# Performance work log

Hardware: AMD Instinct MI355X
Metric: run time of the kernel (lower is better)

The kernel has to match this reference:

```python
import jax, jax.numpy as jnp
import numpy as np
from jax import lax


def _conv(x, w):
    # x: [B,H,W,C], w: [kh,kw,Cin,Cout], stride 1, 'same' padding
    return lax.conv_general_dilated(x, w, window_strides=(1, 1), padding='SAME',
                                    dimension_numbers=('NHWC', 'HWIO', 'NHWC'))


def setup_inputs() -> dict:
    key = jax.random.key(0)
    ks = jax.random.split(key, 4)
    B, T, H, W, Cin, F = 16, 5, 256, 256, 3, 8
    return {
        'input_tensor': jax.random.normal(ks[0], (B, T, H, W, Cin), jnp.float32),
        'kernel': jax.random.normal(ks[1], (3, 3, Cin, 4 * F), jnp.float32) * 0.1,
        'recurrent_kernel': jax.random.normal(ks[2], (3, 3, F, 4 * F), jnp.float32) * 0.1,
        'bias': jnp.zeros((4 * F,), jnp.float32),
        'gamma': jnp.ones((F,), jnp.float32),
        'beta': jnp.zeros((F,), jnp.float32),
        'moving_mean': jnp.zeros((F,), jnp.float32),
        'moving_var': jnp.ones((F,), jnp.float32),
        'dense_w': jax.random.normal(ks[3], (F, 2), jnp.float32) * 0.1,
        'dense_b': jnp.zeros((2,), jnp.float32),
    }


def reference(input_tensor, kernel, recurrent_kernel, bias, gamma, beta,
              moving_mean, moving_var, dense_w, dense_b):
    B, T, H, W, Cin = input_tensor.shape
    F = recurrent_kernel.shape[2]
    xs = jnp.moveaxis(input_tensor, 1, 0)  # [T,B,H,W,Cin] time-major for scan
    h0 = jnp.zeros((B, H, W, F), input_tensor.dtype)

    def step(carry, x_t):
        h, c = carry
        # fused 4-gate pre-activations, Keras gate order: i, f, c(g), o
        z = _conv(x_t, kernel) + _conv(h, recurrent_kernel) + bias
        i, f, g, o = jnp.split(z, 4, axis=-1)
        i = jax.nn.sigmoid(i)
        f = jax.nn.sigmoid(f)
        g = jnp.tanh(g)
        o = jax.nn.sigmoid(o)
        c = f * c + i * g
        h = o * jnp.tanh(c)
        return (h, c), None

    (h, _), _ = lax.scan(step, (h0, h0), xs)  # return_sequences=False -> last h

    # BatchNormalization (inference, Keras eps=1e-3)
    eps = 1e-3
    x = (h - moving_mean) * lax.rsqrt(moving_var + eps) * gamma + beta
    # LeakyReLU, Keras default alpha=0.3
    x = jnp.where(x >= 0, x, 0.3 * x)
    # Dense(2) over channel dim
    return jnp.einsum('bhwf,fk->bhwk', x, dense_w) + dense_b
```

## Files before the change

### kernel.cpp

```cpp
#include <hip/hip_runtime.h>


#define BB  16
#define TT  5
#define HH  256
#define WW  256
#define CIN 3
#define FF  8
#define GG  32

#define TW  32
#define THT 16
#define LW  34
#define LH  18
#define NG  8

#define SW  30
#define SH  14
#define NPX 9
#define NPY 19

#define LOG2E 1.44269504088896340736f

typedef _Float16 half8  __attribute__((ext_vector_type(8)));
typedef _Float16 half4  __attribute__((ext_vector_type(4)));
typedef _Float16 half2t __attribute__((ext_vector_type(2)));
typedef float    floatx4 __attribute__((ext_vector_type(4)));

__device__ __forceinline__ float frcp(float x) { return __builtin_amdgcn_rcpf(x); }
__device__ __forceinline__ float sig2(float z)  { return frcp(1.0f + __builtin_amdgcn_exp2f(z)); }
__device__ __forceinline__ float tanh2(float z) { return 1.0f - 2.0f * frcp(1.0f + __builtin_amdgcn_exp2f(z)); }

__device__ __forceinline__ int clampi(int v, int lo, int hi) {
    return v < lo ? lo : (v > hi ? hi : v);
}

#define MFMA(A, B, C) __builtin_amdgcn_mfma_f32_16x16x32_f16((A), (B), (C), 0, 0, 0)

#define GATES(ACC0, ACC1, C0, C1, CN0, CN1, HN0, HN1)                         \
  float CN0, CN1, HN0, HN1;                                                   \
  {                                                                           \
    float s0 = lo8 ? ACC0[2] : ACC0[0]; float r0 = __shfl_xor(s0, 8, 64);     \
    float s1 = lo8 ? ACC0[3] : ACC0[1]; float r1 = __shfl_xor(s1, 8, 64);     \
    float s2 = lo8 ? ACC1[2] : ACC1[0]; float r2 = __shfl_xor(s2, 8, 64);     \
    float s3 = lo8 ? ACC1[3] : ACC1[1]; float r3 = __shfl_xor(s3, 8, 64);     \
    const float zi0 = lo8 ? ACC0[0] : r0, zi1 = lo8 ? ACC0[1] : r1;           \
    const float zf0 = lo8 ? r0 : ACC0[2], zf1 = lo8 ? r1 : ACC0[3];           \
    const float zg0 = lo8 ? ACC1[0] : r2, zg1 = lo8 ? ACC1[1] : r3;           \
    const float zo0 = lo8 ? r2 : ACC1[2], zo1 = lo8 ? r3 : ACC1[3];           \
    const float ii0 = sig2(zi0), ff0 = sig2(zf0), gg0 = tanh2(zg0), oo0 = sig2(zo0); \
    CN0 = ff0 * (C0) + ii0 * gg0;                                             \
    HN0 = oo0 * tanh2(CN0 * (2.0f * LOG2E));                                  \
    const float ii1 = sig2(zi1), ff1 = sig2(zf1), gg1 = tanh2(zg1), oo1 = sig2(zo1); \
    CN1 = ff1 * (C1) + ii1 * gg1;                                             \
    HN1 = oo1 * tanh2(CN1 * (2.0f * LOG2E));                                  \
  }

__global__ void build_frags(const float* __restrict__ wk,
                            const float* __restrict__ wr,
                            _Float16* __restrict__ blob) {
    const int lane = threadIdx.x & 63;
    const int quad = lane >> 4, nlo = lane & 15;
    for (int chunk = 0; chunk < 5; ++chunk) {
        for (int nh = 0; nh < 2; ++nh) {
            const int n = nh * 16 + nlo;
            const float scale = (n >= 16 && n < 24) ? (2.0f * LOG2E) : (-LOG2E);
            const int frag = chunk * 2 + nh;
            _Float16* dhi = blob + ((size_t)frag * 64 + lane) * 8;
            _Float16* dlo = (chunk >= 2)
                ? blob + ((size_t)(10 + (chunk - 2) * 2 + nh) * 64 + lane) * 8
                : nullptr;
            for (int j = 0; j < 8; ++j) {
                const int k = quad * 8 + j;
                float w = 0.0f;
                if (chunk == 0) {
                    int tap = k >> 2, ci = k & 3;
                    if (ci < 3) w = wk[(tap * 3 + ci) * GG + n];
                } else if (chunk == 1) {
                    if (quad == 0 && j < 3) w = wk[(8 * 3 + j) * GG + n];
                } else {
                    int c = chunk - 2;
                    int tap = c * 4 + quad, ci = j;
                    if (tap < 9) w = wr[(tap * FF + ci) * GG + n];
                }
                w *= scale;
                _Float16 wh = (_Float16)w;
                dhi[j] = wh;
                if (dlo) dlo[j] = (_Float16)(w - (float)wh);
            }
        }
    }
}

template <int FIRSTPAIR>
__global__ __launch_bounds__(256) void lstm_pair(
    const float* __restrict__ xg,
    int t,
    const _Float16* __restrict__ blob,
    const float* __restrict__ bias,
    const _Float16* __restrict__ hin,
    _Float16* __restrict__ hout,
    const _Float16* __restrict__ cin,
    _Float16* __restrict__ cout)
{
    __shared__ half8 hls1[LH * LW];
    __shared__ half4 xls1[LH * LW];
    __shared__ half4 xls2[THT * TW];
    __shared__ __align__(16) _Float16 hls2[THT * TW * FF];

    const int tid  = threadIdx.x;
    const int lane = tid & 63, wave = tid >> 6;
    const int quad = lane >> 4, nlo = lane & 15;
    const bool lo8 = (nlo < 8);
    const int fc = nlo & 7;
    const int m0 = quad * 4 + (lo8 ? 0 : 2);

    const int bx = blockIdx.x, by = blockIdx.y, b = blockIdx.z;
    const int x0 = bx * SW - 1, y0 = by * SH - 1;

    half8 bfh[10], bfl[6];
#pragma unroll
    for (int i = 0; i < 10; ++i)
        bfh[i] = *(const half8*)(blob + ((size_t)i * 64 + lane) * 8);
#pragma unroll
    for (int i = 0; i < 6; ++i)
        bfl[i] = *(const half8*)(blob + ((size_t)(10 + i) * 64 + lane) * 8);

    const float bv0 = bias[nlo] * (-LOG2E);
    const float bv1 = bias[16 + nlo] * (lo8 ? 2.0f * LOG2E : -LOG2E);

    float xr1[3][3];
    bool  xin1[3];
#pragma unroll
    for (int k = 0; k < 3; ++k) {
        const int l = tid + k * 256;
        const bool in = (l < LH * LW);
        xin1[k] = in;
        int r = l / LW, c = l - r * LW;
        int gy = y0 - 1 + r, gx = x0 - 1 + c;
        const bool inb = in && (unsigned)gy < HH && (unsigned)gx < WW;
        const float* p = xg + (((size_t)(b * TT + t) * HH + gy) * WW + gx) * CIN;
        xr1[k][0] = inb ? p[0] : 0.0f;
        xr1[k][1] = inb ? p[1] : 0.0f;
        xr1[k][2] = inb ? p[2] : 0.0f;
    }
    float xr2[2][3];
#pragma unroll
    for (int k = 0; k < 2; ++k) {
        const int l = tid + k * 256;
        int r = l >> 5, c = l & 31;
        int gy = y0 + r, gx = x0 + c;
        const bool inb = (unsigned)gy < HH && (unsigned)gx < WW;
        const float* p = xg + (((size_t)(b * TT + t + 1) * HH + gy) * WW + gx) * CIN;
        xr2[k][0] = inb ? p[0] : 0.0f;
        xr2[k][1] = inb ? p[1] : 0.0f;
        xr2[k][2] = inb ? p[2] : 0.0f;
    }
    half8 hr[3];
    if (!FIRSTPAIR) {
#pragma unroll
        for (int k = 0; k < 3; ++k) {
            const int l = tid + k * 256;
            const bool in = (l < LH * LW);
            int r = l / LW, c = l - r * LW;
            int gy = y0 - 1 + r, gx = x0 - 1 + c;
            const bool inb = in && (unsigned)gy < HH && (unsigned)gx < WW;
            half8 v = {(_Float16)0, (_Float16)0, (_Float16)0, (_Float16)0,
                       (_Float16)0, (_Float16)0, (_Float16)0, (_Float16)0};
            if (inb) v = *(const half8*)(hin + ((size_t)(b * HH + gy) * WW + gx) * FF);
            hr[k] = v;
        }
    }
    half2t cpre[NG];
    if (!FIRSTPAIR) {
#pragma unroll
        for (int g = 0; g < NG; ++g) {
            const int lr  = wave * 4 + (g >> 1);
            const int gx0 = (g & 1) * 16;
            const int gy  = y0 + lr;
            const int gxa = x0 + gx0 + m0;
            const bool iny = (unsigned)gy < HH;
            half2t cv; cv.x = (_Float16)0; cv.y = (_Float16)0;
            const _Float16* cp = cin + ((size_t)(b * HH + gy) * WW + gxa) * FF + fc;
            if (iny && (unsigned)gxa < WW)       cv.x = cp[0];
            if (iny && (unsigned)(gxa + 1) < WW) cv.y = cp[FF];
            cpre[g] = cv;
        }
    }

#pragma unroll
    for (int k = 0; k < 3; ++k) {
        if (xin1[k]) {
            half4 vh;
            vh.x = (_Float16)xr1[k][0];
            vh.y = (_Float16)xr1[k][1];
            vh.z = (_Float16)xr1[k][2];
            vh.w = (_Float16)0;
            xls1[tid + k * 256] = vh;
        }
    }
#pragma unroll
    for (int k = 0; k < 2; ++k) {
        half4 vh;
        vh.x = (_Float16)xr2[k][0];
        vh.y = (_Float16)xr2[k][1];
        vh.z = (_Float16)xr2[k][2];
        vh.w = (_Float16)0;
        xls2[tid + k * 256] = vh;
    }
    if (!FIRSTPAIR) {
#pragma unroll
        for (int k = 0; k < 3; ++k)
            if (xin1[k]) hls1[tid + k * 256] = hr[k];
    }
    __syncthreads();

    half2t creg[NG];
#pragma unroll
    for (int g = 0; g < NG; ++g) {
        const int lr  = wave * 4 + (g >> 1);
        const int gx0 = (g & 1) * 16;
        const int lc  = gx0 + nlo;

        const int t0 = 2 * quad, t1 = t0 + 1;
        half4 p  = xls1[(lr + t0 / 3) * LW + lc + t0 % 3];
        half4 q  = xls1[(lr + t1 / 3) * LW + lc + t1 % 3];
        half4 s8 = xls1[(lr + 2) * LW + lc + 2];
        half8 a_xA = (half8){p.x, p.y, p.z, p.w, q.x, q.y, q.z, q.w};
        half8 a_xB = (half8){s8.x, s8.y, s8.z, s8.w, s8.x, s8.y, s8.z, s8.w};

        floatx4 acc0 = {bv0, bv0, bv0, bv0};
        floatx4 acc1 = {bv1, bv1, bv1, bv1};
        acc0 = MFMA(a_xA, bfh[0], acc0);  acc1 = MFMA(a_xA, bfh[1], acc1);
        acc0 = MFMA(a_xB, bfh[2], acc0);  acc1 = MFMA(a_xB, bfh[3], acc1);
        if (!FIRSTPAIR) {
#pragma unroll
            for (int c = 0; c < 3; ++c) {
                int tap = c * 4 + quad;
                if (tap > 8) tap = 8;
                half8 ah = hls1[(lr + tap / 3) * LW + lc + tap % 3];
                acc0 = MFMA(ah, bfh[4 + c * 2], acc0);
                acc1 = MFMA(ah, bfh[5 + c * 2], acc1);
                acc0 = MFMA(ah, bfl[c * 2 + 0], acc0);
                acc1 = MFMA(ah, bfl[c * 2 + 1], acc1);
            }
        }

        const float c0 = FIRSTPAIR ? 0.0f : (float)cpre[g].x;
        const float c1 = FIRSTPAIR ? 0.0f : (float)cpre[g].y;
        GATES(acc0, acc1, c0, c1, cn0, cn1, hn0, hn1);

        half2t cc; cc.x = (_Float16)cn0; cc.y = (_Float16)cn1;
        creg[g] = cc;

        const int gy   = y0 + lr;
        const int colm = gx0 + m0;
        const int gxa  = x0 + colm;
        const bool iny = (unsigned)gy < HH;
        _Float16 h0v = (_Float16)hn0, h1v = (_Float16)hn1;
        if (!(iny && (unsigned)gxa < WW))       h0v = (_Float16)0;
        if (!(iny && (unsigned)(gxa + 1) < WW)) h1v = (_Float16)0;
        hls2[(lr * TW + colm) * FF + fc]     = h0v;
        hls2[(lr * TW + colm + 1) * FF + fc] = h1v;
    }
    __syncthreads();

#pragma unroll
    for (int g = 0; g < NG; ++g) {
        const int lr  = wave * 4 + (g >> 1);
        const int gx0 = (g & 1) * 16;
        const int lc  = gx0 + nlo;

        const int t0 = 2 * quad, t1 = t0 + 1;
        half4 p  = xls2[clampi(lr + t0 / 3 - 1, 0, THT - 1) * TW + clampi(lc + t0 % 3 - 1, 0, TW - 1)];
        half4 q  = xls2[clampi(lr + t1 / 3 - 1, 0, THT - 1) * TW + clampi(lc + t1 % 3 - 1, 0, TW - 1)];
        half4 s8 = xls2[clampi(lr + 1, 0, THT - 1) * TW + clampi(lc + 1, 0, TW - 1)];
        half8 a_xA = (half8){p.x, p.y, p.z, p.w, q.x, q.y, q.z, q.w};
        half8 a_xB = (half8){s8.x, s8.y, s8.z, s8.w, s8.x, s8.y, s8.z, s8.w};

        floatx4 acc0 = {bv0, bv0, bv0, bv0};
        floatx4 acc1 = {bv1, bv1, bv1, bv1};
        acc0 = MFMA(a_xA, bfh[0], acc0);  acc1 = MFMA(a_xA, bfh[1], acc1);
        acc0 = MFMA(a_xB, bfh[2], acc0);  acc1 = MFMA(a_xB, bfh[3], acc1);
#pragma unroll
        for (int c = 0; c < 3; ++c) {
            int tap = c * 4 + quad;
            if (tap > 8) tap = 8;
            const int rr = clampi(lr + tap / 3 - 1, 0, THT - 1);
            const int cc = clampi(lc + tap % 3 - 1, 0, TW - 1);
            half8 ah = *(const half8*)(hls2 + (rr * TW + cc) * FF);
            acc0 = MFMA(ah, bfh[4 + c * 2], acc0);
            acc1 = MFMA(ah, bfh[5 + c * 2], acc1);
            acc0 = MFMA(ah, bfl[c * 2 + 0], acc0);
            acc1 = MFMA(ah, bfl[c * 2 + 1], acc1);
        }

        GATES(acc0, acc1, (float)creg[g].x, (float)creg[g].y, cn0, cn1, hn0, hn1);

        const int gy   = y0 + lr;
        const int colm = gx0 + m0;
        const int gxa  = x0 + colm;
        const bool rowok = (lr >= 1) && (lr <= SH) && ((unsigned)gy < HH);
        const bool c0ok = rowok && (colm >= 1) && (colm <= SW) && ((unsigned)gxa < WW);
        const bool c1ok = rowok && (colm + 1 <= SW) && ((unsigned)(gxa + 1) < WW);
        const size_t base = ((size_t)(b * HH + gy) * WW + gxa) * FF + fc;
        if (c0ok) {
            hout[base] = (_Float16)hn0;
            cout[base] = (_Float16)cn0;
        }
        if (c1ok) {
            hout[base + FF] = (_Float16)hn1;
            cout[base + FF] = (_Float16)cn1;
        }
    }
}

__global__ __launch_bounds__(256) void lstm_last(
    const float* __restrict__ xg,
    const _Float16* __restrict__ blob,
    const float* __restrict__ bias,
    const _Float16* __restrict__ hin,
    const _Float16* __restrict__ cin,
    const float* __restrict__ gamma, const float* __restrict__ beta,
    const float* __restrict__ mean,  const float* __restrict__ var,
    const float* __restrict__ dw,    const float* __restrict__ db,
    float* __restrict__ out)
{
    __shared__ half8 hls[LH * LW];
    __shared__ half4 xls[LH * LW];

    const int tid  = threadIdx.x;
    const int lane = tid & 63, wave = tid >> 6;
    const int quad = lane >> 4, nlo = lane & 15;
    const bool lo8 = (nlo < 8);
    const int fc = nlo & 7;
    const int m0 = quad * 4 + (lo8 ? 0 : 2);
    const int bx = blockIdx.x, by = blockIdx.y, b = blockIdx.z;
    const int t = TT - 1;

    half8 bfh[10], bfl[6];
#pragma unroll
    for (int i = 0; i < 10; ++i)
        bfh[i] = *(const half8*)(blob + ((size_t)i * 64 + lane) * 8);
#pragma unroll
    for (int i = 0; i < 6; ++i)
        bfl[i] = *(const half8*)(blob + ((size_t)(10 + i) * 64 + lane) * 8);

    const float bv0 = bias[nlo] * (-LOG2E);
    const float bv1 = bias[16 + nlo] * (lo8 ? 2.0f * LOG2E : -LOG2E);

    float xr[3][3];
    bool  xin[3];
#pragma unroll
    for (int k = 0; k < 3; ++k) {
        const int l = tid + k * 256;
        const bool in = (l < LH * LW);
        xin[k] = in;
        int r = l / LW, c = l - r * LW;
        int gy = by * THT + r - 1, gx = bx * TW + c - 1;
        const bool inb = in && (unsigned)gy < HH && (unsigned)gx < WW;
        const float* p = xg + (((size_t)(b * TT + t) * HH + gy) * WW + gx) * CIN;
        xr[k][0] = inb ? p[0] : 0.0f;
        xr[k][1] = inb ? p[1] : 0.0f;
        xr[k][2] = inb ? p[2] : 0.0f;
    }
    half8 hr[3];
#pragma unroll
    for (int k = 0; k < 3; ++k) {
        const int l = tid + k * 256;
        const bool in = (l < LH * LW);
        int r = l / LW, c = l - r * LW;
        int gy = by * THT + r - 1, gx = bx * TW + c - 1;
        const bool inb = in && (unsigned)gy < HH && (unsigned)gx < WW;
        half8 v = {(_Float16)0, (_Float16)0, (_Float16)0, (_Float16)0,
                   (_Float16)0, (_Float16)0, (_Float16)0, (_Float16)0};
        if (inb) v = *(const half8*)(hin + ((size_t)(b * HH + gy) * WW + gx) * FF);
        hr[k] = v;
    }
    half2t cpre[NG];
#pragma unroll
    for (int g = 0; g < NG; ++g) {
        const int lr  = wave * 4 + (g >> 1);
        const int gx0 = (g & 1) * 16;
        const int gy  = by * THT + lr;
        const int gxa = bx * TW + gx0 + m0;
        const _Float16* cp = cin + ((size_t)(b * HH + gy) * WW + gxa) * FF + fc;
        half2t cv; cv.x = cp[0]; cv.y = cp[FF];
        cpre[g] = cv;
    }

#pragma unroll
    for (int k = 0; k < 3; ++k) {
        if (xin[k]) {
            half4 vh;
            vh.x = (_Float16)xr[k][0];
            vh.y = (_Float16)xr[k][1];
            vh.z = (_Float16)xr[k][2];
            vh.w = (_Float16)0;
            xls[tid + k * 256] = vh;
            hls[tid + k * 256] = hr[k];
        }
    }
    __syncthreads();

    const float bn_s = gamma[fc] * rsqrtf(var[fc] + 1e-3f);
    const float bn_b = beta[fc] - mean[fc] * bn_s;
    const float dw0 = dw[fc * 2 + 0], dw1 = dw[fc * 2 + 1];
    const float db0 = db[0], db1 = db[1];

#pragma unroll
    for (int g = 0; g < NG; ++g) {
        const int lr  = wave * 4 + (g >> 1);
        const int gx0 = (g & 1) * 16;
        const int lc  = gx0 + nlo;

        const int t0 = 2 * quad, t1 = t0 + 1;
        half4 p  = xls[(lr + t0 / 3) * LW + lc + t0 % 3];
        half4 q  = xls[(lr + t1 / 3) * LW + lc + t1 % 3];
        half4 s8 = xls[(lr + 2) * LW + lc + 2];
        half8 a_xA = (half8){p.x, p.y, p.z, p.w, q.x, q.y, q.z, q.w};
        half8 a_xB = (half8){s8.x, s8.y, s8.z, s8.w, s8.x, s8.y, s8.z, s8.w};

        floatx4 acc0 = {bv0, bv0, bv0, bv0};
        floatx4 acc1 = {bv1, bv1, bv1, bv1};
        acc0 = MFMA(a_xA, bfh[0], acc0);  acc1 = MFMA(a_xA, bfh[1], acc1);
        acc0 = MFMA(a_xB, bfh[2], acc0);  acc1 = MFMA(a_xB, bfh[3], acc1);
#pragma unroll
        for (int c = 0; c < 3; ++c) {
            int tap = c * 4 + quad;
            if (tap > 8) tap = 8;
            half8 ah = hls[(lr + tap / 3) * LW + lc + tap % 3];
            acc0 = MFMA(ah, bfh[4 + c * 2], acc0);
            acc1 = MFMA(ah, bfh[5 + c * 2], acc1);
            acc0 = MFMA(ah, bfl[c * 2 + 0], acc0);
            acc1 = MFMA(ah, bfl[c * 2 + 1], acc1);
        }

        GATES(acc0, acc1, (float)cpre[g].x, (float)cpre[g].y, cn0, cn1, hn0, hn1);
        (void)cn0; (void)cn1;

        const int gy = by * THT + lr;
        float y0 = bn_s * hn0 + bn_b; y0 = (y0 >= 0.f) ? y0 : 0.3f * y0;
        float y1 = bn_s * hn1 + bn_b; y1 = (y1 >= 0.f) ? y1 : 0.3f * y1;
        float p00 = y0 * dw0, p01 = y0 * dw1;
        float p10 = y1 * dw0, p11 = y1 * dw1;
#pragma unroll
        for (int m = 1; m <= 4; m <<= 1) {
            p00 += __shfl_xor(p00, m, 64);
            p01 += __shfl_xor(p01, m, 64);
            p10 += __shfl_xor(p10, m, 64);
            p11 += __shfl_xor(p11, m, 64);
        }
        const int j = nlo & 7;
        if (j < 4) {
            const int px = m0 + (j >> 1);
            const int k  = j & 1;
            float val = (j == 0 ? p00 : j == 1 ? p01 : j == 2 ? p10 : p11)
                        + (k ? db1 : db0);
            out[((size_t)(b * HH + gy) * WW + bx * TW + gx0 + px) * 2 + k] = val;
        }
    }
}

extern "C" void kernel_launch(void* const* d_in, const int* in_sizes, int n_in,
                              void* d_out, int out_size, void* d_ws, size_t ws_size,
                              hipStream_t stream) {
    const float* x     = (const float*)d_in[0];
    const float* wk    = (const float*)d_in[1];
    const float* wr    = (const float*)d_in[2];
    const float* bias  = (const float*)d_in[3];
    const float* gamma = (const float*)d_in[4];
    const float* beta  = (const float*)d_in[5];
    const float* mean  = (const float*)d_in[6];
    const float* var   = (const float*)d_in[7];
    const float* dw    = (const float*)d_in[8];
    const float* db    = (const float*)d_in[9];
    float* out = (float*)d_out;

    const size_t state = (size_t)BB * HH * WW * FF;
    _Float16* blob = (_Float16*)d_ws;
    _Float16* hA = (_Float16*)((char*)d_ws + 32768);
    _Float16* hB = hA + state;
    _Float16* cA = hB + state;
    _Float16* cB = cA + state;

    build_frags<<<1, 64, 0, stream>>>(wk, wr, blob);

    dim3 pgrid(NPX, NPY, BB), block(256);
    lstm_pair<1><<<pgrid, block, 0, stream>>>(x, 0, blob, bias,
                                              nullptr, hA, nullptr, cA);
    lstm_pair<0><<<pgrid, block, 0, stream>>>(x, 2, blob, bias,
                                              hA, hB, cA, cB);
    dim3 lgrid(WW / TW, HH / THT, BB);
    lstm_last<<<lgrid, block, 0, stream>>>(x, blob, bias, hB, cB,
                                           gamma, beta, mean, var, dw, db, out);
}
```

Baseline: 292.4 us.

## Switch LSTM kernels to single-wave 16x16 tiles and drop block barriers

Each fused LSTM kernel now uses one 64-lane wave per block instead of four waves. Tiles shrink from 32x16 to 16x16, with an 18x18 haloed load and a stride of 14 for the pair kernels. Because all LDS producers and consumers sit in one wave, the __syncthreads calls are removed, and each lane walks 16 rows sequentially with the cell state kept in registers. The cost is a larger share of redundant halo recomputation and many more small blocks. It also leans on in-wave LDS ordering, with no explicit barrier or fence.

New measurement: 287.7 us. No clear change (-1.6%).

```diff
diff --git a/kernel.cpp b/kernel.cpp
--- a/kernel.cpp
+++ b/kernel.cpp
@@ -9,16 +9,10 @@
 #define FF  8
 #define GG  32
 
-#define TW  32
-#define THT 16
-#define LW  34
-#define LH  18
-#define NG  8
-
-#define SW  30
-#define SH  14
-#define NPX 9
-#define NPY 19
+#define TIW 16
+#define TLW 18
+#define STR 14
+#define NPT 19
 
 #define LOG2E 1.44269504088896340736f
 
@@ -93,7 +87,7 @@
 }
 
 template <int FIRSTPAIR>
-__global__ __launch_bounds__(256) void lstm_pair(
+__global__ __launch_bounds__(64) void lstm_pair(
     const float* __restrict__ xg,
     int t,
     const _Float16* __restrict__ blob,
@@ -103,20 +97,19 @@
     const _Float16* __restrict__ cin,
     _Float16* __restrict__ cout)
 {
-    __shared__ half8 hls1[LH * LW];
-    __shared__ half4 xls1[LH * LW];
-    __shared__ half4 xls2[THT * TW];
-    __shared__ __align__(16) _Float16 hls2[THT * TW * FF];
-
-    const int tid  = threadIdx.x;
-    const int lane = tid & 63, wave = tid >> 6;
+    __shared__ half4 xls1[TLW * TLW];
+    __shared__ half8 hls1[TLW * TLW];
+    __shared__ half4 xls2[TIW * TIW];
+    __shared__ __align__(16) _Float16 hls2[TIW * TIW * FF];
+
+    const int lane = threadIdx.x;
     const int quad = lane >> 4, nlo = lane & 15;
     const bool lo8 = (nlo < 8);
     const int fc = nlo & 7;
     const int m0 = quad * 4 + (lo8 ? 0 : 2);
 
     const int bx = blockIdx.x, by = blockIdx.y, b = blockIdx.z;
-    const int x0 = bx * SW - 1, y0 = by * SH - 1;
+    const int x0 = bx * STR - 1, y0 = by * STR - 1;
 
     half8 bfh[10], bfl[6];
 #pragma unroll
@@ -129,103 +122,133 @@
     const float bv0 = bias[nlo] * (-LOG2E);
     const float bv1 = bias[16 + nlo] * (lo8 ? 2.0f * LOG2E : -LOG2E);
 
-    float xr1[3][3];
-    bool  xin1[3];
-#pragma unroll
-    for (int k = 0; k < 3; ++k) {
-        const int l = tid + k * 256;
-        const bool in = (l < LH * LW);
-        xin1[k] = in;
-        int r = l / LW, c = l - r * LW;
-        int gy = y0 - 1 + r, gx = x0 - 1 + c;
+    float xr1[6][3];
+#pragma unroll
+    for (int k = 0; k < 6; ++k) {
+        const int l = lane + k * 64;
+        const bool in = (l < TLW * TLW);
+        const int r = l / TLW, c = l - r * TLW;
+        const int gy = y0 - 1 + r, gx = x0 - 1 + c;
         const bool inb = in && (unsigned)gy < HH && (unsigned)gx < WW;
         const float* p = xg + (((size_t)(b * TT + t) * HH + gy) * WW + gx) * CIN;
         xr1[k][0] = inb ? p[0] : 0.0f;
         xr1[k][1] = inb ? p[1] : 0.0f;
         xr1[k][2] = inb ? p[2] : 0.0f;
     }
-    float xr2[2][3];
-#pragma unroll
-    for (int k = 0; k < 2; ++k) {
-        const int l = tid + k * 256;
-        int r = l >> 5, c = l & 31;
-        int gy = y0 + r, gx = x0 + c;
+    half8 hr[6];
+    if (!FIRSTPAIR) {
+#pragma unroll
+        for (int k = 0; k < 6; ++k) {
+            const int l = lane + k * 64;
+            const bool in = (l < TLW * TLW);
+            const int r = l / TLW, c = l - r * TLW;
+            const int gy = y0 - 1 + r, gx = x0 - 1 + c;
+            const bool inb = in && (unsigned)gy < HH && (unsigned)gx < WW;
+            half8 v = {(_Float16)0, (_Float16)0, (_Float16)0, (_Float16)0,
+                       (_Float16)0, (_Float16)0, (_Float16)0, (_Float16)0};
+            if (inb) v = *(const half8*)(hin + ((size_t)(b * HH + gy) * WW + gx) * FF);
+            hr[k] = v;
+        }
+    }
+    half2t creg[TIW];
+#pragma unroll
+    for (int g = 0; g < TIW; ++g) {
+        half2t cv; cv.x = (_Float16)0; cv.y = (_Float16)0;
+        if (!FIRSTPAIR) {
+            const int gy = y0 + g, gxa = x0 + m0;
+            const bool iny = (unsigned)gy < HH;
+            const _Float16* cp = cin + ((size_t)(b * HH + gy) * WW + gxa) * FF + fc;
+            if (iny && (unsigned)gxa < WW)       cv.x = cp[0];
+            if (iny && (unsigned)(gxa + 1) < WW) cv.y = cp[FF];
+        }
+        creg[g] = cv;
+    }
+
+#pragma unroll
+    for (int k = 0; k < 6; ++k) {
+        const int l = lane + k * 64;
+        if (l < TLW * TLW) {
+            half4 vh;
+            vh.x = (_Float16)xr1[k][0];
+            vh.y = (_Float16)xr1[k][1];
+            vh.z = (_Float16)xr1[k][2];
+            vh.w = (_Float16)0;
+            xls1[l] = vh;
+            if (!FIRSTPAIR) hls1[l] = hr[k];
+        }
+    }
+
+    float xr2[4][3];
+#pragma unroll
+    for (int k = 0; k < 4; ++k) {
+        const int l = lane + k * 64;
+        const int r = l >> 4, c = l & 15;
+        const int gy = y0 + r, gx = x0 + c;
         const bool inb = (unsigned)gy < HH && (unsigned)gx < WW;
         const float* p = xg + (((size_t)(b * TT + t + 1) * HH + gy) * WW + gx) * CIN;
         xr2[k][0] = inb ? p[0] : 0.0f;
         xr2[k][1] = inb ? p[1] : 0.0f;
         xr2[k][2] = inb ? p[2] : 0.0f;
     }
-    half8 hr[3];
-    if (!FIRSTPAIR) {
-#pragma unroll
-        for (int k = 0; k < 3; ++k) {
-            const int l = tid + k * 256;
-            const bool in = (l < LH * LW);
-            int r = l / LW, c = l - r * LW;
-            int gy = y0 - 1 + r, gx = x0 - 1 + c;
-            const bool inb = in && (unsigned)gy < HH && (unsigned)gx < WW;
-            half8 v = {(_Float16)0, (_Float16)0, (_Float16)0, (_Float16)0,
-                       (_Float16)0, (_Float16)0, (_Float16)0, (_Float16)0};
-            if (inb) v = *(const half8*)(hin + ((size_t)(b * HH + gy) * WW + gx) * FF);
-            hr[k] = v;
-        }
-    }
-    half2t cpre[NG];
-    if (!FIRSTPAIR) {
-#pragma unroll
-        for (int g = 0; g < NG; ++g) {
-            const int lr  = wave * 4 + (g >> 1);
-            const int gx0 = (g & 1) * 16;
-            const int gy  = y0 + lr;
-            const int gxa = x0 + gx0 + m0;
-            const bool iny = (unsigned)gy < HH;
-            half2t cv; cv.x = (_Float16)0; cv.y = (_Float16)0;
-            const _Float16* cp = cin + ((size_t)(b * HH + gy) * WW + gxa) * FF + fc;
-            if (iny && (unsigned)gxa < WW)       cv.x = cp[0];
-            if (iny && (unsigned)(gxa + 1) < WW) cv.y = cp[FF];
-            cpre[g] = cv;
-        }
-    }
-
-#pragma unroll
-    for (int k = 0; k < 3; ++k) {
-        if (xin1[k]) {
-            half4 vh;
-            vh.x = (_Float16)xr1[k][0];
-            vh.y = (_Float16)xr1[k][1];
-            vh.z = (_Float16)xr1[k][2];
-            vh.w = (_Float16)0;
-            xls1[tid + k * 256] = vh;
-        }
-    }
-#pragma unroll
-    for (int k = 0; k < 2; ++k) {
+
+#pragma unroll
+    for (int g = 0; g < TIW; ++g) {
+        const int t0 = 2 * quad, t1 = t0 + 1;
+        half4 p  = xls1[(g + t0 / 3) * TLW + nlo + t0 % 3];
+        half4 q  = xls1[(g + t1 / 3) * TLW + nlo + t1 % 3];
+        half4 s8 = xls1[(g + 2) * TLW + nlo + 2];
+        half8 a_xA = (half8){p.x, p.y, p.z, p.w, q.x, q.y, q.z, q.w};
+        half8 a_xB = (half8){s8.x, s8.y, s8.z, s8.w, s8.x, s8.y, s8.z, s8.w};
+
+        floatx4 acc0 = {bv0, bv0, bv0, bv0};
+        floatx4 acc1 = {bv1, bv1, bv1, bv1};
+        acc0 = MFMA(a_xA, bfh[0], acc0);  acc1 = MFMA(a_xA, bfh[1], acc1);
+        acc0 = MFMA(a_xB, bfh[2], acc0);  acc1 = MFMA(a_xB, bfh[3], acc1);
+        if (!FIRSTPAIR) {
+#pragma unroll
+            for (int c = 0; c < 3; ++c) {
+                int tap = c * 4 + quad;
+                if (tap > 8) tap = 8;
+                half8 ah = hls1[(g + tap / 3) * TLW + nlo + tap % 3];
+                acc0 = MFMA(ah, bfh[4 + c * 2], acc0);
+                acc1 = MFMA(ah, bfh[5 + c * 2], acc1);
+                acc0 = MFMA(ah, bfl[c * 2 + 0], acc0);
+                acc1 = MFMA(ah, bfl[c * 2 + 1], acc1);
+            }
+        }
+
+        GATES(acc0, acc1, (float)creg[g].x, (float)creg[g].y, cn0, cn1, hn0, hn1);
+
+        half2t cc; cc.x = (_Float16)cn0; cc.y = (_Float16)cn1;
+        creg[g] = cc;
+
+        const int gy  = y0 + g;
+        const int gxa = x0 + m0;
+        const bool iny = (unsigned)gy < HH;
+        _Float16 h0v = (_Float16)hn0, h1v = (_Float16)hn1;
+        if (!(iny && (unsigned)gxa < WW))       h0v = (_Float16)0;
+        if (!(iny && (unsigned)(gxa + 1) < WW)) h1v = (_Float16)0;
+        hls2[(g * TIW + m0) * FF + fc]     = h0v;
+        hls2[(g * TIW + m0 + 1) * FF + fc] = h1v;
+    }
+
+#pragma unroll
+    for (int k = 0; k < 4; ++k) {
+        const int l = lane + k * 64;
         half4 vh;
         vh.x = (_Float16)xr2[k][0];
         vh.y = (_Float16)xr2[k][1];
         vh.z = (_Float16)xr2[k][2];
         vh.w = (_Float16)0;
-        xls2[tid + k * 256] = vh;
-    }
-    if (!FIRSTPAIR) {
-#pragma unroll
-        for (int k = 0; k < 3; ++k)
-            if (xin1[k]) hls1[tid + k * 256] = hr[k];
-    }
-    __syncthreads();
-
-    half2t creg[NG];
-#pragma unroll
-    for (int g = 0; g < NG; ++g) {
-        const int lr  = wave * 4 + (g >> 1);
-        const int gx0 = (g & 1) * 16;
-        const int lc  = gx0 + nlo;
-
+        xls2[l] = vh;
+    }
+
+#pragma unroll
+    for (int g = 0; g < TIW; ++g) {
         const int t0 = 2 * quad, t1 = t0 + 1;
-        half4 p  = xls1[(lr + t0 / 3) * LW + lc + t0 % 3];
-        half4 q  = xls1[(lr + t1 / 3) * LW + lc + t1 % 3];
-        half4 s8 = xls1[(lr + 2) * LW + lc + 2];
+        half4 p  = xls2[clampi(g + t0 / 3 - 1, 0, TIW - 1) * TIW + clampi(nlo + t0 % 3 - 1, 0, TIW - 1)];
+        half4 q  = xls2[clampi(g + t1 / 3 - 1, 0, TIW - 1) * TIW + clampi(nlo + t1 % 3 - 1, 0, TIW - 1)];
+        half4 s8 = xls2[clampi(g + 1, 0, TIW - 1) * TIW + clampi(nlo + 1, 0, TIW - 1)];
         half8 a_xA = (half8){p.x, p.y, p.z, p.w, q.x, q.y, q.z, q.w};
         half8 a_xB = (half8){s8.x, s8.y, s8.z, s8.w, s8.x, s8.y, s8.z, s8.w};
 
@@ -233,62 +256,13 @@
         floatx4 acc1 = {bv1, bv1, bv1, bv1};
         acc0 = MFMA(a_xA, bfh[0], acc0);  acc1 = MFMA(a_xA, bfh[1], acc1);
         acc0 = MFMA(a_xB, bfh[2], acc0);  acc1 = MFMA(a_xB, bfh[3], acc1);
-        if (!FIRSTPAIR) {
-#pragma unroll
-            for (int c = 0; c < 3; ++c) {
-                int tap = c * 4 + quad;
-                if (tap > 8) tap = 8;
-                half8 ah = hls1[(lr + tap / 3) * LW + lc + tap % 3];
-                acc0 = MFMA(ah, bfh[4 + c * 2], acc0);
-                acc1 = MFMA(ah, bfh[5 + c * 2], acc1);
-                acc0 = MFMA(ah, bfl[c * 2 + 0], acc0);
-                acc1 = MFMA(ah, bfl[c * 2 + 1], acc1);
-            }
-        }
-
-        const float c0 = FIRSTPAIR ? 0.0f : (float)cpre[g].x;
-        const float c1 = FIRSTPAIR ? 0.0f : (float)cpre[g].y;
-        GATES(acc0, acc1, c0, c1, cn0, cn1, hn0, hn1);
-
-        half2t cc; cc.x = (_Float16)cn0; cc.y = (_Float16)cn1;
-        creg[g] = cc;
-
-        const int gy   = y0 + lr;
-        const int colm = gx0 + m0;
-        const int gxa  = x0 + colm;
-        const bool iny = (unsigned)gy < HH;
-        _Float16 h0v = (_Float16)hn0, h1v = (_Float16)hn1;
-        if (!(iny && (unsigned)gxa < WW))       h0v = (_Float16)0;
-        if (!(iny && (unsigned)(gxa + 1) < WW)) h1v = (_Float16)0;
-        hls2[(lr * TW + colm) * FF + fc]     = h0v;
-        hls2[(lr * TW + colm + 1) * FF + fc] = h1v;
-    }
-    __syncthreads();
-
-#pragma unroll
-    for (int g = 0; g < NG; ++g) {
-        const int lr  = wave * 4 + (g >> 1);
-        const int gx0 = (g & 1) * 16;
-        const int lc  = gx0 + nlo;
-
-        const int t0 = 2 * quad, t1 = t0 + 1;
-        half4 p  = xls2[clampi(lr + t0 / 3 - 1, 0, THT - 1) * TW + clampi(lc + t0 % 3 - 1, 0, TW - 1)];
-        half4 q  = xls2[clampi(lr + t1 / 3 - 1, 0, THT - 1) * TW + clampi(lc + t1 % 3 - 1, 0, TW - 1)];
-        half4 s8 = xls2[clampi(lr + 1, 0, THT - 1) * TW + clampi(lc + 1, 0, TW - 1)];
-        half8 a_xA = (half8){p.x, p.y, p.z, p.w, q.x, q.y, q.z, q.w};
-        half8 a_xB = (half8){s8.x, s8.y, s8.z, s8.w, s8.x, s8.y, s8.z, s8.w};
-
-        floatx4 acc0 = {bv0, bv0, bv0, bv0};
-        floatx4 acc1 = {bv1, bv1, bv1, bv1};
-        acc0 = MFMA(a_xA, bfh[0], acc0);  acc1 = MFMA(a_xA, bfh[1], acc1);
-        acc0 = MFMA(a_xB, bfh[2], acc0);  acc1 = MFMA(a_xB, bfh[3], acc1);
 #pragma unroll
         for (int c = 0; c < 3; ++c) {
             int tap = c * 4 + quad;
             if (tap > 8) tap = 8;
-            const int rr = clampi(lr + tap / 3 - 1, 0, THT - 1);
-            const int cc = clampi(lc + tap % 3 - 1, 0, TW - 1);
-            half8 ah = *(const half8*)(hls2 + (rr * TW + cc) * FF);
+            const int rr = clampi(g + tap / 3 - 1, 0, TIW - 1);
+            const int cc = clampi(nlo + tap % 3 - 1, 0, TIW - 1);
+            half8 ah = *(const half8*)(hls2 + (rr * TIW + cc) * FF);
             acc0 = MFMA(ah, bfh[4 + c * 2], acc0);
             acc1 = MFMA(ah, bfh[5 + c * 2], acc1);
             acc0 = MFMA(ah, bfl[c * 2 + 0], acc0);
@@ -297,15 +271,14 @@
 
         GATES(acc0, acc1, (float)creg[g].x, (float)creg[g].y, cn0, cn1, hn0, hn1);
 
-        const int gy   = y0 + lr;
-        const int colm = gx0 + m0;
-        const int gxa  = x0 + colm;
-        const bool rowok = (lr >= 1) && (lr <= SH) && ((unsigned)gy < HH);
-        const bool c0ok = rowok && (colm >= 1) && (colm <= SW) && ((unsigned)gxa < WW);
-        const bool c1ok = rowok && (colm + 1 <= SW) && ((unsigned)(gxa + 1) < WW);
+        const int gy  = y0 + g;
+        const int gxa = x0 + m0;
+        const bool rowok = (g >= 1) && (g <= STR) && ((unsigned)gy < HH);
+        const bool c0ok = rowok && (m0 >= 1) && (m0 <= STR) && ((unsigned)gxa < WW);
+        const bool c1ok = rowok && (m0 + 1 <= STR) && ((unsigned)(gxa + 1) < WW);
         const size_t base = ((size_t)(b * HH + gy) * WW + gxa) * FF + fc;
         if (c0ok) {
-            hout[base] = (_Float16)hn0;
+            hout[base] = (_Float16)cn0, hout[base] = (_Float16)hn0;
             cout[base] = (_Float16)cn0;
         }
         if (c1ok) {
@@ -315,7 +288,7 @@
     }
 }
 
-__global__ __launch_bounds__(256) void lstm_last(
+__global__ __launch_bounds__(64) void lstm_last(
     const float* __restrict__ xg,
     const _Float16* __restrict__ blob,
     const float* __restrict__ bias,
@@ -326,16 +299,16 @@
     const float* __restrict__ dw,    const float* __restrict__ db,
     float* __restrict__ out)
 {
-    __shared__ half8 hls[LH * LW];
-    __shared__ half4 xls[LH * LW];
-
-    const int tid  = threadIdx.x;
-    const int lane = tid & 63, wave = tid >> 6;
+    __shared__ half4 xls1[TLW * TLW];
+    __shared__ half8 hls1[TLW * TLW];
+
+    const int lane = threadIdx.x;
     const int quad = lane >> 4, nlo = lane & 15;
     const bool lo8 = (nlo < 8);
     const int fc = nlo & 7;
     const int m0 = quad * 4 + (lo8 ? 0 : 2);
     const int bx = blockIdx.x, by = blockIdx.y, b = blockIdx.z;
+    const int x0 = bx * TIW, y0 = by * TIW;
     const int t = TT - 1;
 
     half8 bfh[10], bfl[6];
@@ -349,59 +322,46 @@
     const float bv0 = bias[nlo] * (-LOG2E);
     const float bv1 = bias[16 + nlo] * (lo8 ? 2.0f * LOG2E : -LOG2E);
 
-    float xr[3][3];
-    bool  xin[3];
-#pragma unroll
-    for (int k = 0; k < 3; ++k) {
-        const int l = tid + k * 256;
-        const bool in = (l < LH * LW);
-        xin[k] = in;
-        int r = l / LW, c = l - r * LW;
-        int gy = by * THT + r - 1, gx = bx * TW + c - 1;
+    float xr1[6][3];
+    half8 hr[6];
+#pragma unroll
+    for (int k = 0; k < 6; ++k) {
+        const int l = lane + k * 64;
+        const bool in = (l < TLW * TLW);
+        const int r = l / TLW, c = l - r * TLW;
+        const int gy = y0 - 1 + r, gx = x0 - 1 + c;
         const bool inb = in && (unsigned)gy < HH && (unsigned)gx < WW;
         const float* p = xg + (((size_t)(b * TT + t) * HH + gy) * WW + gx) * CIN;
-        xr[k][0] = inb ? p[0] : 0.0f;
-        xr[k][1] = inb ? p[1] : 0.0f;
-        xr[k][2] = inb ? p[2] : 0.0f;
-    }
-    half8 hr[3];
-#pragma unroll
-    for (int k = 0; k < 3; ++k) {
-        const int l = tid + k * 256;
-        const bool in = (l < LH * LW);
-        int r = l / LW, c = l - r * LW;
-        int gy = by * THT + r - 1, gx = bx * TW + c - 1;
-        const bool inb = in && (unsigned)gy < HH && (unsigned)gx < WW;
+        xr1[k][0] = inb ? p[0] : 0.0f;
+        xr1[k][1] = inb ? p[1] : 0.0f;
+        xr1[k][2] = inb ? p[2] : 0.0f;
         half8 v = {(_Float16)0, (_Float16)0, (_Float16)0, (_Float16)0,
                    (_Float16)0, (_Float16)0, (_Float16)0, (_Float16)0};
         if (inb) v = *(const half8*)(hin + ((size_t)(b * HH + gy) * WW + gx) * FF);
         hr[k] = v;
     }
-    half2t cpre[NG];
-#pragma unroll
-    for (int g = 0; g < NG; ++g) {
-        const int lr  = wave * 4 + (g >> 1);
-        const int gx0 = (g & 1) * 16;
-        const int gy  = by * THT + lr;
-        const int gxa = bx * TW + gx0 + m0;
+    half2t creg[TIW];
+#pragma unroll
+    for (int g = 0; g < TIW; ++g) {
+        const int gy = y0 + g, gxa = x0 + m0;
         const _Float16* cp = cin + ((size_t)(b * HH + gy) * WW + gxa) * FF + fc;
         half2t cv; cv.x = cp[0]; cv.y = cp[FF];
-        cpre[g] = cv;
-    }
-
-#pragma unroll
-    for (int k = 0; k < 3; ++k) {
-        if (xin[k]) {
+        creg[g] = cv;
+    }
+
+#pragma unroll
+    for (int k = 0; k < 6; ++k) {
+        const int l = lane + k * 64;
+        if (l < TLW * TLW) {
             half4 vh;
-            vh.x = (_Float16)xr[k][0];
-            vh.y = (_Float16)xr[k][1];
-            vh.z = (_Float16)xr[k][2];
+            vh.x = (_Float16)xr1[k][0];
+            vh.y = (_Float16)xr1[k][1];
+            vh.z = (_Float16)xr1[k][2];
             vh.w = (_Float16)0;
-            xls[tid + k * 256] = vh;
-            hls[tid + k * 256] = hr[k];
-        }
-    }
-    __syncthreads();
+            xls1[l] = vh;
+            hls1[l] = hr[k];
+        }
+    }
 
     const float bn_s = gamma[fc] * rsqrtf(var[fc] + 1e-3f);
     const float bn_b = beta[fc] - mean[fc] * bn_s;
@@ -409,15 +369,11 @@
     const float db0 = db[0], db1 = db[1];
 
 #pragma unroll
-    for (int g = 0; g < NG; ++g) {
-        const int lr  = wave * 4 + (g >> 1);
-        const int gx0 = (g & 1) * 16;
-        const int lc  = gx0 + nlo;
-
+    for (int g = 0; g < TIW; ++g) {
         const int t0 = 2 * quad, t1 = t0 + 1;
-        half4 p  = xls[(lr + t0 / 3) * LW + lc + t0 % 3];
-        half4 q  = xls[(lr + t1 / 3) * LW + lc + t1 % 3];
-        half4 s8 = xls[(lr + 2) * LW + lc + 2];
+        half4 p  = xls1[(g + t0 / 3) * TLW + nlo + t0 % 3];
+        half4 q  = xls1[(g + t1 / 3) * TLW + nlo + t1 % 3];
+        half4 s8 = xls1[(g + 2) * TLW + nlo + 2];
         half8 a_xA = (half8){p.x, p.y, p.z, p.w, q.x, q.y, q.z, q.w};
         half8 a_xB = (half8){s8.x, s8.y, s8.z, s8.w, s8.x, s8.y, s8.z, s8.w};
 
@@ -429,21 +385,21 @@
         for (int c = 0; c < 3; ++c) {
             int tap = c * 4 + quad;
             if (tap > 8) tap = 8;
-            half8 ah = hls[(lr + tap / 3) * LW + lc + tap % 3];
+            half8 ah = hls1[(g + tap / 3) * TLW + nlo + tap % 3];
             acc0 = MFMA(ah, bfh[4 + c * 2], acc0);
             acc1 = MFMA(ah, bfh[5 + c * 2], acc1);
             acc0 = MFMA(ah, bfl[c * 2 + 0], acc0);
             acc1 = MFMA(ah, bfl[c * 2 + 1], acc1);
         }
 
-        GATES(acc0, acc1, (float)cpre[g].x, (float)cpre[g].y, cn0, cn1, hn0, hn1);
+        GATES(acc0, acc1, (float)creg[g].x, (float)creg[g].y, cn0, cn1, hn0, hn1);
         (void)cn0; (void)cn1;
 
-        const int gy = by * THT + lr;
-        float y0 = bn_s * hn0 + bn_b; y0 = (y0 >= 0.f) ? y0 : 0.3f * y0;
-        float y1 = bn_s * hn1 + bn_b; y1 = (y1 >= 0.f) ? y1 : 0.3f * y1;
-        float p00 = y0 * dw0, p01 = y0 * dw1;
-        float p10 = y1 * dw0, p11 = y1 * dw1;
+        const int gy = y0 + g;
+        float y0v = bn_s * hn0 + bn_b; y0v = (y0v >= 0.f) ? y0v : 0.3f * y0v;
+        float y1v = bn_s * hn1 + bn_b; y1v = (y1v >= 0.f) ? y1v : 0.3f * y1v;
+        float p00 = y0v * dw0, p01 = y0v * dw1;
+        float p10 = y1v * dw0, p11 = y1v * dw1;
 #pragma unroll
         for (int m = 1; m <= 4; m <<= 1) {
             p00 += __shfl_xor(p00, m, 64);
@@ -457,7 +413,7 @@
             const int k  = j & 1;
             float val = (j == 0 ? p00 : j == 1 ? p01 : j == 2 ? p10 : p11)
                         + (k ? db1 : db0);
-            out[((size_t)(b * HH + gy) * WW + bx * TW + gx0 + px) * 2 + k] = val;
+            out[((size_t)(b * HH + gy) * WW + x0 + px) * 2 + k] = val;
         }
     }
 }
@@ -486,12 +442,12 @@
 
     build_frags<<<1, 64, 0, stream>>>(wk, wr, blob);
 
-    dim3 pgrid(NPX, NPY, BB), block(256);
+    dim3 pgrid(NPT, NPT, BB), block(64);
     lstm_pair<1><<<pgrid, block, 0, stream>>>(x, 0, blob, bias,
                                               nullptr, hA, nullptr, cA);
     lstm_pair<0><<<pgrid, block, 0, stream>>>(x, 2, blob, bias,
                                               hA, hB, cA, cB);
-    dim3 lgrid(WW / TW, HH / THT, BB);
+    dim3 lgrid(HH / TIW, WW / TIW, BB);
     lstm_last<<<lgrid, block, 0, stream>>>(x, blob, bias, hB, cB,
                                            gamma, beta, mean, var, dw, db, out);
 }
```
